# Optimization experiments

Hardware: AMD Instinct MI355X
Metric: run time of the kernel (lower is better)

Reference implementation:

```python
import jax, jax.numpy as jnp
import numpy as np
from jax import lax


def conv(x, w, b, stride, pad):
    # x: [B,C,H,W], w: [O,I,kh,kw] (torch layout)
    y = lax.conv_general_dilated(x, w, (stride, stride), ((pad, pad), (pad, pad)),
                                 dimension_numbers=('NCHW', 'OIHW', 'NCHW'))
    return y + b[None, :, None, None]


def convT(x, w, b, stride, pad):
    # torch ConvTranspose2d weight layout [in, out, kh, kw]
    k = w.shape[2]
    wf = jnp.flip(w, (2, 3)).transpose(1, 0, 2, 3)  # -> [out, in, kh, kw]
    p = k - 1 - pad
    y = lax.conv_general_dilated(x, wf, (1, 1), ((p, p), (p, p)),
                                 lhs_dilation=(stride, stride),
                                 dimension_numbers=('NCHW', 'OIHW', 'NCHW'))
    return y + b[None, :, None, None]


def resblock(x, wa, ba, wb, bb):
    h = conv(jax.nn.relu(x), wa, ba, 1, 1)   # 3x3
    h2 = conv(jax.nn.relu(h), wb, bb, 1, 0)  # 1x1
    return x + h2


def vqvae_forward(x, e1_w, e1_b, e2_w, e2_b, e3_w, e3_b,
                  er1a_w, er1a_b, er1b_w, er1b_b, er2a_w, er2a_b, er2b_w, er2b_b,
                  codebook,
                  d1_w, d1_b, dr1a_w, dr1a_b, dr1b_w, dr1b_b,
                  dr2a_w, dr2a_b, dr2b_w, dr2b_b,
                  dt1_w, dt1_b, dt2_w, dt2_b):
    # encoder
    h = jax.nn.relu(conv(x, e1_w, e1_b, 2, 1))
    h = jax.nn.relu(conv(h, e2_w, e2_b, 2, 1))
    h = conv(h, e3_w, e3_b, 1, 1)
    h = resblock(h, er1a_w, er1a_b, er1b_w, er1b_b)
    ze = resblock(h, er2a_w, er2a_b, er2b_w, er2b_b)  # [B,C,H,W]
    # VQ: nearest codebook vector per spatial location (squared L2)
    zef = ze.transpose(0, 2, 3, 1)  # [B,H,W,C]
    # ||z - e||^2 = ||z||^2 - 2 z.e + ||e||^2 (same argmin as explicit broadcast)
    d = (jnp.sum(zef * zef, -1, keepdims=True)
         - 2.0 * jnp.einsum('bhwc,kc->bhwk', zef, codebook)
         + jnp.sum(codebook * codebook, -1))  # [B,H,W,K]
    idx = jnp.argmin(d, -1)                    # [B,H,W]
    zq = codebook[idx].transpose(0, 3, 1, 2)   # [B,C,H,W]
    # straight-through estimator
    dec_in = ze + lax.stop_gradient(zq - ze)
    # decoder
    g = conv(dec_in, d1_w, d1_b, 1, 1)
    g = resblock(g, dr1a_w, dr1a_b, dr1b_w, dr1b_b)
    g = resblock(g, dr2a_w, dr2a_b, dr2b_w, dr2b_b)
    g = jax.nn.relu(convT(g, dt1_w, dt1_b, 2, 1))
    x_hat = convT(g, dt2_w, dt2_b, 2, 1)
    return x_hat, ze, zq


def setup_inputs() -> dict:
    key = jax.random.key(0)
    ks = iter(jax.random.split(key, 64))
    C, K = 128, 512

    def w(shape, scale=0.02):
        return jax.random.normal(next(ks), shape, jnp.float32) * scale

    inp = {}
    inp['x'] = jax.random.normal(next(ks), (16, 3, 256, 256), jnp.float32)
    inp['e1_w'] = w((C, 3, 4, 4)); inp['e1_b'] = w((C,))
    inp['e2_w'] = w((C, C, 4, 4)); inp['e2_b'] = w((C,))
    inp['e3_w'] = w((C, C, 3, 3)); inp['e3_b'] = w((C,))
    inp['er1a_w'] = w((C, C, 3, 3)); inp['er1a_b'] = w((C,))
    inp['er1b_w'] = w((C, C, 1, 1)); inp['er1b_b'] = w((C,))
    inp['er2a_w'] = w((C, C, 3, 3)); inp['er2a_b'] = w((C,))
    inp['er2b_w'] = w((C, C, 1, 1)); inp['er2b_b'] = w((C,))
    inp['codebook'] = jax.random.uniform(next(ks), (K, C), jnp.float32, -1.0 / K, 1.0 / K)
    inp['d1_w'] = w((C, C, 3, 3)); inp['d1_b'] = w((C,))
    inp['dr1a_w'] = w((C, C, 3, 3)); inp['dr1a_b'] = w((C,))
    inp['dr1b_w'] = w((C, C, 1, 1)); inp['dr1b_b'] = w((C,))
    inp['dr2a_w'] = w((C, C, 3, 3)); inp['dr2a_b'] = w((C,))
    inp['dr2b_w'] = w((C, C, 1, 1)); inp['dr2b_b'] = w((C,))
    inp['dt1_w'] = w((C, C, 4, 4)); inp['dt1_b'] = w((C,))   # ConvTranspose [in,out,kh,kw]
    inp['dt2_w'] = w((C, 3, 4, 4)); inp['dt2_b'] = w((3,))
    return inp


def reference(x, e1_w, e1_b, e2_w, e2_b, e3_w, e3_b,
              er1a_w, er1a_b, er1b_w, er1b_b, er2a_w, er2a_b, er2b_w, er2b_b,
              codebook,
              d1_w, d1_b, dr1a_w, dr1a_b, dr1b_w, dr1b_b,
              dr2a_w, dr2a_b, dr2b_w, dr2b_b,
              dt1_w, dt1_b, dt2_w, dt2_b):
    return vqvae_forward(x, e1_w, e1_b, e2_w, e2_b, e3_w, e3_b,
                         er1a_w, er1a_b, er1b_w, er1b_b, er2a_w, er2a_b, er2b_w, er2b_b,
                         codebook,
                         d1_w, d1_b, dr1a_w, dr1a_b, dr1b_w, dr1b_b,
                         dr2a_w, dr2a_b, dr2b_w, dr2b_b,
                         dt1_w, dt1_b, dt2_w, dt2_b)
```

## Files before the change

### kernel.cpp

```cpp
#include <hip/hip_runtime.h>
#include <stdint.h>

typedef unsigned short u16;
typedef __attribute__((ext_vector_type(8))) short short8;
typedef __attribute__((ext_vector_type(4))) float floatx4;

#define RS66  (66*128)
#define IS66  (66*66*128)
#define RS130 (130*128)
#define IS130 (130*130*128)

__device__ __forceinline__ float bf2f(u16 h) {
  union { unsigned u; float f; } v; v.u = ((unsigned)h) << 16; return v.f;
}
__device__ __forceinline__ u16 f2bf(float f) {
  union { float f; unsigned u; } v; v.f = f;
  unsigned r = v.u + 0x7FFFu + ((v.u >> 16) & 1u);
  return (u16)(r >> 16);
}
__device__ __forceinline__ void gl_lds16(const void* g, void* l) {
  __builtin_amdgcn_global_load_lds(
      (const __attribute__((address_space(1))) void*)(uintptr_t)g,
      (__attribute__((address_space(3))) void*)(uintptr_t)l, 16, 0, 0);
}
__device__ __forceinline__ unsigned fkey(float f) {
  unsigned u = __float_as_uint(f);
  return (u & 0x80000000u) ? ~u : (u | 0x80000000u);
}

struct Taps { int n; unsigned dh2; unsigned dw2; };

__global__ __launch_bounds__(256) void conv_mfma(
    const u16* __restrict__ in, int inRS, int inIS, int si,
    const u16* __restrict__ wt, const float* __restrict__ bias, Taps tp,
    u16* __restrict__ out, int outRS, int outIS, int so, int oh0, int ow0,
    const u16* __restrict__ res, u16* __restrict__ out2, int reluMain,
    float* __restrict__ zeFc, u16* __restrict__ zeBFc, int multi)
{
  __shared__ u16 lA[2][8192];
  __shared__ u16 lB[2][8192];
  const int tid = threadIdx.x;
  const int w = tid >> 6, lane = tid & 63, quad = lane >> 4, l16 = lane & 15;
  const int wm = w >> 1, wn = w & 1;
  const int blockM = blockIdx.x << 7;

  unsigned dh2 = tp.dh2, dw2 = tp.dw2;
  if (multi) {
    const int cls = blockIdx.y;
    dh2 = (tp.dh2 >> (8*cls)) & 0xffu;
    dw2 = (tp.dw2 >> (8*cls)) & 0xffu;
    wt += cls << 16;
    oh0 = cls >> 1; ow0 = cls & 1;
  }

  const int swz = (tid & 7) ^ ((tid >> 3) & 7);
  const u16* gA[4]; const u16* gB[4];
#pragma unroll
  for (int i=0;i<4;i++) {
    const int pg = blockM + i*32 + (tid >> 3);
    const int b = pg >> 12, mo = (pg >> 6) & 63, no = pg & 63;
    gA[i] = in + b*inIS + si*mo*inRS + si*no*128 + swz*8;
    gB[i] = wt + (i*32 + (tid >> 3))*128 + swz*8;
  }
  const int ldsOff = w*512;

  floatx4 zz = {0.f,0.f,0.f,0.f};
  floatx4 acc[4][4];
#pragma unroll
  for (int i=0;i<4;i++)
#pragma unroll
    for (int j=0;j<4;j++) acc[i][j] = zz;

  const int NCH = tp.n << 1;
  auto issue = [&](int ci, int buf) {
    const int t = ci >> 1, kc = ci & 1;
    const int dh = (int)((dh2 >> (2*t)) & 3u) - 1;
    const int dw = (int)((dw2 >> (2*t)) & 3u) - 1;
    const int aoff = dh*inRS + dw*128 + kc*64;
    const int boff = (t << 14) + kc*64;
#pragma unroll
    for (int i=0;i<4;i++) {
      gl_lds16(gA[i] + aoff, &lA[buf][i*2048 + ldsOff]);
      gl_lds16(gB[i] + boff, &lB[buf][i*2048 + ldsOff]);
    }
  };

  issue(0, 0);
  for (int ci = 0; ci < NCH; ++ci) {
    __syncthreads();
    if (ci + 1 < NCH) issue(ci + 1, (ci + 1) & 1);
    const u16* bufA = lA[ci & 1];
    const u16* bufB = lB[ci & 1];
#pragma unroll
    for (int kk=0; kk<2; ++kk) {
      short8 af[4], bfr[4];
#pragma unroll
      for (int s=0;s<4;s++) {
        const int row = wm*64 + s*16 + l16;
        af[s]  = *(const short8*)&bufA[row*64 + (((kk*4 + quad) ^ (l16 & 7)) << 3)];
      }
#pragma unroll
      for (int s=0;s<4;s++) {
        const int row = wn*64 + s*16 + l16;
        bfr[s] = *(const short8*)&bufB[row*64 + (((kk*4 + quad) ^ (l16 & 7)) << 3)];
      }
#pragma unroll
      for (int i=0;i<4;i++)
#pragma unroll
        for (int j=0;j<4;j++)
          acc[i][j] = __builtin_amdgcn_mfma_f32_16x16x32_bf16(af[i], bfr[j], acc[i][j], 0, 0, 0);
    }
  }

  float bv[4];
#pragma unroll
  for (int j=0;j<4;j++) bv[j] = bias[wn*64 + j*16 + l16];

#pragma unroll
  for (int i=0;i<4;i++) {
#pragma unroll
    for (int r=0;r<4;r++) {
      const int p = blockM + wm*64 + i*16 + quad*4 + r;
      const int bb = p >> 12, mo = (p >> 6) & 63, no = p & 63;
      const int ob = bb*outIS + (so*mo + oh0)*outRS + (so*no + ow0)*128;
#pragma unroll
      for (int j=0;j<4;j++) {
        const int n = wn*64 + j*16 + l16;
        float v = acc[i][j][r] + bv[j];
        if (res)  v += bf2f(res[ob + n]);
        if (out)  out[ob + n]  = f2bf(reluMain ? fmaxf(v, 0.f) : v);
        if (out2) out2[ob + n] = f2bf(fmaxf(v, 0.f));
        if (zeFc) {
          zeFc[((size_t)p << 7) + n] = v;
          zeBFc[((size_t)p << 7) + n] = f2bf(v);
        }
      }
    }
  }
}

__global__ __launch_bounds__(256) void vq_score(
    const u16* __restrict__ zeBF, const u16* __restrict__ cbBF,
    const float* __restrict__ cbn, unsigned long long* __restrict__ minbuf)
{
  __shared__ u16 lA[4096];
  __shared__ u16 lB[4096];
  const int tid = threadIdx.x;
  const int w = tid >> 6, lane = tid & 63, quad = lane >> 4, l16 = lane & 15;
  const int wm = w >> 1, wn = w & 1;
  const int q = tid & 3, p0 = tid >> 2;
  const int blockM = blockIdx.x << 7;
  const int nb = blockIdx.y;
  const u16* gA0 = zeBF + ((blockM + p0) << 7) + q*8;
  const u16* gA1 = gA0 + (64 << 7);
  const u16* gB0 = cbBF + ((nb*128 + p0) << 7) + q*8;
  const u16* gB1 = gB0 + (64 << 7);
  u16* lsA0 = lA + w*512; u16* lsA1 = lsA0 + 2048;
  u16* lsB0 = lB + w*512; u16* lsB1 = lsB0 + 2048;

  floatx4 zz = {0.f,0.f,0.f,0.f};
  floatx4 acc[4][4];
#pragma unroll
  for (int i=0;i<4;i++)
#pragma unroll
    for (int j=0;j<4;j++) acc[i][j] = zz;

#pragma unroll
  for (int kc = 0; kc < 4; ++kc) {
    __syncthreads();
    gl_lds16(gA0 + kc*32, lsA0);
    gl_lds16(gA1 + kc*32, lsA1);
    gl_lds16(gB0 + kc*32, lsB0);
    gl_lds16(gB1 + kc*32, lsB1);
    __syncthreads();
    short8 af[4], bfr[4];
#pragma unroll
    for (int s=0;s<4;s++) af[s]  = *(const short8*)&lA[(wm*64 + s*16 + l16)*32 + quad*8];
#pragma unroll
    for (int s=0;s<4;s++) bfr[s] = *(const short8*)&lB[(wn*64 + s*16 + l16)*32 + quad*8];
#pragma unroll
    for (int i=0;i<4;i++)
#pragma unroll
      for (int j=0;j<4;j++)
        acc[i][j] = __builtin_amdgcn_mfma_f32_16x16x32_bf16(af[i], bfr[j], acc[i][j], 0, 0, 0);
  }

  float cn[4];
#pragma unroll
  for (int j=0;j<4;j++) cn[j] = cbn[nb*128 + wn*64 + j*16 + l16];

#pragma unroll
  for (int i=0;i<4;i++) {
#pragma unroll
    for (int r=0;r<4;r++) {
      const int p = blockM + wm*64 + i*16 + quad*4 + r;
      unsigned long long best = 0xFFFFFFFFFFFFFFFFull;
#pragma unroll
      for (int j=0;j<4;j++) {
        const int n = nb*128 + wn*64 + j*16 + l16;
        float v = cn[j] - acc[i][j][r];
        unsigned long long pk = ((unsigned long long)fkey(v) << 32) | (unsigned)n;
        if (pk < best) best = pk;
      }
#pragma unroll
      for (int d=1; d<16; d<<=1) {
        unsigned long long o = __shfl_xor(best, d, 64);
        if (o < best) best = o;
      }
      if (l16 == 0) atomicMin(minbuf + p, best);
    }
  }
}

__global__ __launch_bounds__(256) void finalize(
    const float* __restrict__ zeFc, const unsigned long long* __restrict__ minb,
    const float* __restrict__ cb, float* __restrict__ outZe, float* __restrict__ outZq,
    u16* __restrict__ zqI)
{
  __shared__ float T[64*129];
  __shared__ int ns[64];
  const int tid = threadIdx.x;
  const int P0 = blockIdx.x << 6;
  const int b = P0 >> 12, hw0 = P0 & 4095;

#pragma unroll
  for (int it=0; it<32; ++it) {
    int e = it*256 + tid;
    int px = e >> 7, c = e & 127;
    T[px*129 + c] = zeFc[((size_t)P0 << 7) + e];
  }
  if (tid < 64) ns[tid] = (int)(unsigned)(minb[P0 + tid] & 0xFFFFFFFFull);
  __syncthreads();

  float* zeB = outZe + (((size_t)b) << 19) + hw0;
  float* zqB = outZq + (((size_t)b) << 19) + hw0;
  const int h = hw0 >> 6;
  u16* zqIB = zqI + b*IS66 + h*RS66;
#pragma unroll
  for (int it=0; it<32; ++it) {
    const int c = it*4 + (tid >> 6);
    const int px = tid & 63;
    zeB[(c << 12) + px] = T[px*129 + c];
    float v = cb[(ns[px] << 7) + c];
    zqB[(c << 12) + px] = v;
    zqIB[px*128 + c] = f2bf(v);
  }
}

__global__ __launch_bounds__(256) void zero_halos(
    u16* big, u16* s0, u16* s1, u16* s2, u16* s3, unsigned long long* minb)
{
  int id = blockIdx.x*256 + threadIdx.x;
  if (id >= 463872) return;
  if (id >= 398336) { minb[id - 398336] = 0xFFFFFFFFFFFFFFFFull; return; }
  u16* base; int H, W;
  if (id < 132096) { base = big; H = 128; W = 128; }
  else {
    id -= 132096;
    int bi = id / 66560;
    id -= bi*66560;
    base = (bi == 0) ? s0 : (bi == 1) ? s1 : (bi == 2) ? s2 : s3;
    H = 64; W = 64;
  }
  int Wp = W+2, Hp = H+2;
  int cv = id & 15; int rest = id >> 4;
  int npx = 2*Wp + 2*H;
  int img = rest / npx; int pix = rest - img*npx;
  int hh, wwp;
  if (pix < Wp) { hh = 0; wwp = pix; }
  else if (pix < 2*Wp) { hh = Hp-1; wwp = pix - Wp; }
  else { int r2 = pix - 2*Wp; hh = 1 + (r2 >> 1); wwp = (r2 & 1) ? (Wp-1) : 0; }
  uint4 zv = {0u,0u,0u,0u};
  *(uint4*)(base + (((size_t)img*Hp + hh)*Wp + wwp)*128 + cv*8) = zv;
}

struct WEnt { const float* src; u16* dst; int O, I, T, mode; };
struct WTab { int n; WEnt e[16]; int cum[17]; };
__global__ __launch_bounds__(256) void prep_w(WTab wt) {
  int id = blockIdx.x*256 + threadIdx.x;
  if (id >= wt.cum[wt.n]) return;
  int k = 0;
  while (id >= wt.cum[k+1]) k++;
  int l = id - wt.cum[k];
  WEnt E = wt.e[k];
  if (E.mode == 0) {
    int i = l % E.I; int rest = l / E.I; int o = rest % E.O; int t = rest / E.O;
    E.dst[l] = f2bf(E.src[(o*E.I + i)*E.T + t]);
  } else if (E.mode == 1) {
    int i = l & 127, o = (l >> 7) & 127, tt = (l >> 14) & 3, cls = l >> 16;
    int th = tt >> 1, tw = tt & 1, po = cls >> 1, pw = cls & 1;
    int kh = po ? (th ? 2 : 0) : (th ? 3 : 1);
    int kw = pw ? (tw ? 2 : 0) : (tw ? 3 : 1);
    E.dst[l] = f2bf(E.src[((i*128 + o)*4 + kh)*4 + kw]);
  } else if (E.mode == 2) {
    E.dst[l] = f2bf(E.src[l]);
  } else if (E.mode == 3) {
    float s = 0.f; const float* r = E.src + l*128;
    for (int c=0;c<128;c++) s += r[c]*r[c];
    ((float*)E.dst)[l] = 0.5f*s;
  } else if (E.mode == 4) {
    int o = l & 127, tap = l >> 7;
    ((float*)E.dst)[l] = E.src[o*48 + tap];
  } else {
    int c = l & 127, n = l >> 7;
    int o = n >> 4, kk = n & 15;
    E.dst[l] = f2bf(E.src[c*48 + o*16 + kk]);
  }
}

__global__ __launch_bounds__(256) void conv_e1(
    const float* __restrict__ x, const float* __restrict__ wT,
    const float* __restrict__ bias, u16* __restrict__ outI)
{
  __shared__ float inS[12*260];
  __shared__ float wS[48*128];
  __shared__ float bS[128];
  const int tid = threadIdx.x;
  const int b = blockIdx.x >> 7, ho = blockIdx.x & 127;

  for (int l = tid; l < 1536; l += 256)
    ((float4*)wS)[l] = ((const float4*)wT)[l];
  if (tid < 128) bS[tid] = bias[tid];
  for (int l = tid; l < 3120; l += 256) {
    int col = l % 260; int rest = l / 260;
    int kh = rest & 3, c = rest >> 2;
    int hi = 2*ho + kh - 1, wi = col - 1;
    float v = 0.f;
    if ((unsigned)hi < 256u && (unsigned)wi < 256u)
      v = x[((b*3 + c) << 16) + (hi << 8) + wi];
    inS[rest*260 + col] = v;
  }
  __syncthreads();

  const int g = tid & 7;
  const int pxg = tid >> 3;
  floatx4 acc[4][4];
  {
    const floatx4* bp = (const floatx4*)&bS[g*16];
    floatx4 b0 = bp[0], b1 = bp[1], b2 = bp[2], b3 = bp[3];
#pragma unroll
    for (int px=0;px<4;px++) { acc[px][0]=b0; acc[px][1]=b1; acc[px][2]=b2; acc[px][3]=b3; }
  }
#pragma unroll
  for (int c=0;c<3;c++)
#pragma unroll
    for (int kh=0;kh<4;kh++) {
      const float* row = &inS[(c*4+kh)*260];
#pragma unroll
      for (int kw=0;kw<4;kw++) {
        const int tap = c*16 + kh*4 + kw;
        const floatx4* wp = (const floatx4*)&wS[tap*128 + g*16];
        floatx4 w0 = wp[0], w1 = wp[1], w2 = wp[2], w3 = wp[3];
#pragma unroll
        for (int px=0;px<4;px++) {
          float xv = row[((pxg*4 + px) << 1) + kw];
          acc[px][0] += xv*w0; acc[px][1] += xv*w1;
          acc[px][2] += xv*w2; acc[px][3] += xv*w3;
        }
      }
    }

  u16* ob = outI + b*IS130 + ho*RS130;
#pragma unroll
  for (int px=0;px<4;px++) {
    const int wo = pxg*4 + px;
    u16* p = ob + wo*128 + g*16;
#pragma unroll
    for (int k=0;k<4;k++) {
      union { u16 u[4]; uint2 v2; } pk;
#pragma unroll
      for (int j=0;j<4;j++) pk.u[j] = f2bf(fmaxf(acc[px][k][j], 0.f));
      *(uint2*)(p + k*4) = pk.v2;
    }
  }
}

__global__ __launch_bounds__(256) void dt2_gemm(
    const u16* __restrict__ inI, const u16* __restrict__ Wb,
    float* __restrict__ cols)
{
  const int tid = threadIdx.x;
  const int w = tid >> 6, lane = tid & 63, quad = lane >> 4, l16 = lane & 15;
  const int pixBase = blockIdx.x*256 + w*64;

  short8 Bf[3][4];
#pragma unroll
  for (int nt=0; nt<3; nt++)
#pragma unroll
    for (int kc=0; kc<4; kc++)
      Bf[nt][kc] = *(const short8*)(Wb + (nt*16 + l16)*128 + kc*32 + quad*8);

  const u16* ap[4];
#pragma unroll
  for (int ms=0; ms<4; ms++) {
    int p = pixBase + ms*16 + l16;
    int b = p >> 14, rem = p & 16383;
    ap[ms] = inI + b*IS130 + (rem >> 7)*RS130 + (rem & 127)*128;
  }

  floatx4 zz = {0.f,0.f,0.f,0.f};
  floatx4 acc[4][3];
#pragma unroll
  for (int ms=0; ms<4; ms++)
#pragma unroll
    for (int nt=0; nt<3; nt++) acc[ms][nt] = zz;

#pragma unroll
  for (int kc=0; kc<4; kc++) {
#pragma unroll
    for (int ms=0; ms<4; ms++) {
      short8 a = *(const short8*)(ap[ms] + kc*32 + quad*8);
#pragma unroll
      for (int nt=0; nt<3; nt++)
        acc[ms][nt] = __builtin_amdgcn_mfma_f32_16x16x32_bf16(a, Bf[nt][kc], acc[ms][nt], 0, 0, 0);
    }
  }

#pragma unroll
  for (int ms=0; ms<4; ms++)
#pragma unroll
    for (int nt=0; nt<3; nt++)
#pragma unroll
      for (int r=0; r<4; r++) {
        int p = pixBase + ms*16 + quad*4 + r;
        cols[(size_t)p*48 + nt*16 + l16] = acc[ms][nt][r];
      }
}

__global__ __launch_bounds__(256) void dt2_gather(
    const float* __restrict__ cols, const float* __restrict__ bias,
    float* __restrict__ xhat)
{
  int id = blockIdx.x*256 + threadIdx.x;
  int b = id >> 16, rem = id & 65535;
  int ho = rem >> 8, wo = rem & 255;
  const int ph = ho & 1, pw = wo & 1;
  const int hi0 = ph ? ((ho+1)>>1) : (ho>>1);
  const int kh0 = ph ? 0 : 1;
  const int wi0 = pw ? ((wo+1)>>1) : (wo>>1);
  const int kw0 = pw ? 0 : 1;
  float a0 = bias[0], a1 = bias[1], a2 = bias[2];
#pragma unroll
  for (int th=0; th<2; th++) {
    const int hi = hi0 - th;
    if ((unsigned)hi >= 128u) continue;
    const int kh = kh0 + 2*th;
#pragma unroll
    for (int tw=0; tw<2; tw++) {
      const int wi = wi0 - tw;
      if ((unsigned)wi >= 128u) continue;
      const int kw = kw0 + 2*tw;
      const float* r = cols + (size_t)((b << 14) + (hi << 7) + wi)*48 + (kh*4 + kw);
      a0 += r[0]; a1 += r[16]; a2 += r[32];
    }
  }
  const int ob = ((b*3) << 16) + (ho << 8) + wo;
  xhat[ob]          = a0;
  xhat[ob + 65536]  = a1;
  xhat[ob + 131072] = a2;
}

extern "C" void kernel_launch(void* const* d_in, const int* in_sizes, int n_in,
                              void* d_out, int out_size, void* d_ws, size_t ws_size,
                              hipStream_t stream)
{
  const float* x     = (const float*)d_in[0];
  const float* e1w   = (const float*)d_in[1];
  const float* e1b   = (const float*)d_in[2];
  const float* e2w   = (const float*)d_in[3];
  const float* e2b   = (const float*)d_in[4];
  const float* e3w   = (const float*)d_in[5];
  const float* e3b   = (const float*)d_in[6];
  const float* er1aw = (const float*)d_in[7];
  const float* er1ab = (const float*)d_in[8];
  const float* er1bw = (const float*)d_in[9];
  const float* er1bb = (const float*)d_in[10];
  const float* er2aw = (const float*)d_in[11];
  const float* er2ab = (const float*)d_in[12];
  const float* er2bw = (const float*)d_in[13];
  const float* er2bb = (const float*)d_in[14];
  const float* cb    = (const float*)d_in[15];
  const float* d1w   = (const float*)d_in[16];
  const float* d1b   = (const float*)d_in[17];
  const float* dr1aw = (const float*)d_in[18];
  const float* dr1ab = (const float*)d_in[19];
  const float* dr1bw = (const float*)d_in[20];
  const float* dr1bb = (const float*)d_in[21];
  const float* dr2aw = (const float*)d_in[22];
  const float* dr2ab = (const float*)d_in[23];
  const float* dr2bw = (const float*)d_in[24];
  const float* dr2bb = (const float*)d_in[25];
  const float* dt1w  = (const float*)d_in[26];
  const float* dt1b  = (const float*)d_in[27];
  const float* dt2w  = (const float*)d_in[28];
  const float* dt2b  = (const float*)d_in[29];
  float* out = (float*)d_out;

  char* ws = (char*)d_ws;
  size_t off = 0;
  auto alloc = [&](size_t bytes) -> void* {
    void* r = ws + off; off += (bytes + 255) & ~(size_t)255; return r;
  };

  u16* BIG = (u16*)alloc((size_t)IS130*16*2);
  u16* S[4];
  for (int i=0;i<4;i++) S[i] = (u16*)alloc((size_t)IS66*16*2);
  unsigned long long* minb = (unsigned long long*)alloc((size_t)65536*8);
  u16* W_e2 = (u16*)alloc(262144*2);
  u16* W9[6]; for (int i=0;i<6;i++) W9[i] = (u16*)alloc(147456*2);
  u16* W1[4]; for (int i=0;i<4;i++) W1[i] = (u16*)alloc(16384*2);
  u16* Wdt1 = (u16*)alloc(262144*2);
  u16* cbBF = (u16*)alloc(65536*2);
  float* cbn = (float*)alloc(512*4);
  float* wsE1 = (float*)alloc(6144*4);
  u16* Wb48 = (u16*)alloc(6144*2);

  u16* BIGi = BIG + RS130 + 128;
  u16* Si[4];
  for (int i=0;i<4;i++) Si[i] = S[i] + RS66 + 128;
  u16* zeBFc = S[1];
  float* zeFc = (float*)BIG;
  float* cols = (float*)S[1];

  zero_halos<<<1812, 256, 0, stream>>>(BIG, S[0], S[1], S[2], S[3], minb);

  WTab wtab; int ne = 0; wtab.cum[0] = 0;
  auto addw = [&](const float* s, u16* d, int O, int I, int T, int m, int items) {
    wtab.e[ne] = {s, d, O, I, T, m};
    wtab.cum[ne+1] = wtab.cum[ne] + items; ne++;
  };
  addw(e2w,   W_e2, 128,128,16,0, 262144);
  addw(e3w,   W9[0],128,128, 9,0, 147456);
  addw(er1aw, W9[1],128,128, 9,0, 147456);
  addw(er2aw, W9[2],128,128, 9,0, 147456);
  addw(d1w,   W9[3],128,128, 9,0, 147456);
  addw(dr1aw, W9[4],128,128, 9,0, 147456);
  addw(dr2aw, W9[5],128,128, 9,0, 147456);
  addw(er1bw, W1[0],128,128, 1,0, 16384);
  addw(er2bw, W1[1],128,128, 1,0, 16384);
  addw(dr1bw, W1[2],128,128, 1,0, 16384);
  addw(dr2bw, W1[3],128,128, 1,0, 16384);
  addw(dt1w,  Wdt1, 0,0,0,1, 262144);
  addw(cb,    cbBF, 0,0,0,2, 65536);
  addw(cb,    (u16*)cbn, 0,0,0,3, 512);
  addw(e1w,   (u16*)wsE1, 0,0,0,4, 6144);
  addw(dt2w,  Wb48, 0,0,0,5, 6144);
  wtab.n = ne;
  prep_w<<<(wtab.cum[ne] + 255)/256, 256, 0, stream>>>(wtab);

  conv_e1<<<2048, 256, 0, stream>>>(x, wsE1, e1b, BIGi);

  Taps t16; t16.n = 16; t16.dh2 = 0; t16.dw2 = 0;
  for (int t=0;t<16;t++) { t16.dh2 |= (unsigned)(t>>2) << (2*t); t16.dw2 |= (unsigned)(t&3) << (2*t); }
  Taps t9; t9.n = 9; t9.dh2 = 0; t9.dw2 = 0;
  for (int t=0;t<9;t++) { t9.dh2 |= (unsigned)(t/3) << (2*t); t9.dw2 |= (unsigned)(t%3) << (2*t); }
  Taps t1x; t1x.n = 1; t1x.dh2 = 1; t1x.dw2 = 1;
  Taps tcm; tcm.n = 4; tcm.dh2 = 0; tcm.dw2 = 0;
  for (int cls=0; cls<4; ++cls) {
    int po = cls >> 1, pw = cls & 1;
    for (int tt=0; tt<4; ++tt) {
      int th = tt >> 1, tw = tt & 1;
      int dh = po ? (th ? 0 : 1) : (th ? -1 : 0);
      int dw = pw ? (tw ? 0 : 1) : (tw ? -1 : 0);
      tcm.dh2 |= (unsigned)(dh+1) << (8*cls + 2*tt);
      tcm.dw2 |= (unsigned)(dw+1) << (8*cls + 2*tt);
    }
  }

  auto conv = [&](const u16* in_, int iRS, int iIS, int si,
                  const u16* w_, const float* b_, Taps tp,
                  u16* o_, int oRS, int oIS, int so, int oh, int ow,
                  const u16* r_, u16* o2, int rl, float* zf, u16* zb) {
    conv_mfma<<<512, 256, 0, stream>>>(in_, iRS, iIS, si, w_, b_, tp,
                                       o_, oRS, oIS, so, oh, ow, r_, o2, rl, zf, zb, 0);
  };

  conv(BIGi, RS130, IS130, 2, W_e2, e2b, t16, Si[0], RS66, IS66, 1,0,0, nullptr, nullptr, 1, nullptr, nullptr);
  conv(Si[0], RS66, IS66, 1, W9[0], e3b, t9, Si[1], RS66, IS66, 1,0,0, nullptr, Si[2], 0, nullptr, nullptr);
  conv(Si[2], RS66, IS66, 1, W9[1], er1ab, t9, Si[0], RS66, IS66, 1,0,0, nullptr, nullptr, 1, nullptr, nullptr);
  conv(Si[0], RS66, IS66, 1, W1[0], er1bb, t1x, Si[3], RS66, IS66, 1,0,0, Si[1], Si[2], 0, nullptr, nullptr);
  conv(Si[2], RS66, IS66, 1, W9[2], er2ab, t9, Si[0], RS66, IS66, 1,0,0, nullptr, nullptr, 1, nullptr, nullptr);
  conv(Si[0], RS66, IS66, 1, W1[1], er2bb, t1x, nullptr, RS66, IS66, 1,0,0, Si[3], nullptr, 0, zeFc, zeBFc);

  vq_score<<<dim3(512,4), 256, 0, stream>>>(zeBFc, cbBF, cbn, minb);
  finalize<<<1024, 256, 0, stream>>>(zeFc, minb, cb, out + 3145728, out + 11534336, Si[2]);

  conv(Si[2], RS66, IS66, 1, W9[3], d1b, t9, Si[0], RS66, IS66, 1,0,0, nullptr, Si[1], 0, nullptr, nullptr);
  conv(Si[1], RS66, IS66, 1, W9[4], dr1ab, t9, Si[2], RS66, IS66, 1,0,0, nullptr, nullptr, 1, nullptr, nullptr);
  conv(Si[2], RS66, IS66, 1, W1[2], dr1bb, t1x, Si[3], RS66, IS66, 1,0,0, Si[0], Si[1], 0, nullptr, nullptr);
  conv(Si[1], RS66, IS66, 1, W9[5], dr2ab, t9, Si[2], RS66, IS66, 1,0,0, nullptr, nullptr, 1, nullptr, nullptr);
  conv(Si[2], RS66, IS66, 1, W1[3], dr2bb, t1x, Si[0], RS66, IS66, 1,0,0, Si[3], nullptr, 0, nullptr, nullptr);

  conv_mfma<<<dim3(512,4), 256, 0, stream>>>(Si[0], RS66, IS66, 1, Wdt1, dt1b, tcm,
                                             BIGi, RS130, IS130, 2, 0, 0,
                                             nullptr, nullptr, 1, nullptr, nullptr, 1);

  dt2_gemm<<<1024, 256, 0, stream>>>(BIGi, Wb48, cols);
  dt2_gather<<<4096, 256, 0, stream>>>(cols, dt2b, out);
}
```

Measured before the change: 693.5 us.

## Load MFMA weight fragments directly to registers and swizzle block order

Weights and codebook are pre-packed in prep_w into an MFMA-fragment-ordered layout, so conv_mfma and vq_score read B operands straight from global memory into registers with a software double buffer instead of staging them through LDS. This halves LDS usage, and launch bounds now ask for 3 blocks per CU. Block indices are remapped so that consecutive blocks are spread across distant M tiles, which is meant to improve cache behaviour across CUs. The cost is that every wave fetches B from global or L2 memory on its own, and more registers are in use for the prefetch.

```diff
diff --git a/kernel.cpp b/kernel.cpp
--- a/kernel.cpp
+++ b/kernel.cpp
@@ -30,7 +30,7 @@
 
 struct Taps { int n; unsigned dh2; unsigned dw2; };
 
-__global__ __launch_bounds__(256) void conv_mfma(
+__global__ __launch_bounds__(256, 3) void conv_mfma(
     const u16* __restrict__ in, int inRS, int inIS, int si,
     const u16* __restrict__ wt, const float* __restrict__ bias, Taps tp,
     u16* __restrict__ out, int outRS, int outIS, int so, int oh0, int ow0,
@@ -38,11 +38,11 @@
     float* __restrict__ zeFc, u16* __restrict__ zeBFc, int multi)
 {
   __shared__ u16 lA[2][8192];
-  __shared__ u16 lB[2][8192];
   const int tid = threadIdx.x;
   const int w = tid >> 6, lane = tid & 63, quad = lane >> 4, l16 = lane & 15;
   const int wm = w >> 1, wn = w & 1;
-  const int blockM = blockIdx.x << 7;
+  const int bx = ((blockIdx.x & 7) << 6) | (blockIdx.x >> 3);
+  const int blockM = bx << 7;
 
   unsigned dh2 = tp.dh2, dw2 = tp.dw2;
   if (multi) {
@@ -54,14 +54,14 @@
   }
 
   const int swz = (tid & 7) ^ ((tid >> 3) & 7);
-  const u16* gA[4]; const u16* gB[4];
+  const u16* gA[4];
 #pragma unroll
   for (int i=0;i<4;i++) {
     const int pg = blockM + i*32 + (tid >> 3);
     const int b = pg >> 12, mo = (pg >> 6) & 63, no = pg & 63;
     gA[i] = in + b*inIS + si*mo*inRS + si*no*128 + swz*8;
-    gB[i] = wt + (i*32 + (tid >> 3))*128 + swz*8;
-  }
+  }
+  const u16* gBf = wt + (wn*64 + l16)*32 + quad*8;
   const int ldsOff = w*512;
 
   floatx4 zz = {0.f,0.f,0.f,0.f};
@@ -71,45 +71,46 @@
 #pragma unroll
     for (int j=0;j<4;j++) acc[i][j] = zz;
 
-  const int NCH = tp.n << 1;
-  auto issue = [&](int ci, int buf) {
+  auto issueA = [&](int ci, int buf) {
     const int t = ci >> 1, kc = ci & 1;
     const int dh = (int)((dh2 >> (2*t)) & 3u) - 1;
     const int dw = (int)((dw2 >> (2*t)) & 3u) - 1;
     const int aoff = dh*inRS + dw*128 + kc*64;
-    const int boff = (t << 14) + kc*64;
-#pragma unroll
-    for (int i=0;i<4;i++) {
+#pragma unroll
+    for (int i=0;i<4;i++)
       gl_lds16(gA[i] + aoff, &lA[buf][i*2048 + ldsOff]);
-      gl_lds16(gB[i] + boff, &lB[buf][i*2048 + ldsOff]);
-    }
-  };
-
-  issue(0, 0);
+  };
+  short8 bX[4], bY[4];
+  auto loadB = [&](int ci, int kk, short8 (&b)[4]) {
+    const u16* p = gBf + ci*8192 + kk*4096;
+#pragma unroll
+    for (int s=0;s<4;s++) b[s] = *(const short8*)(p + s*512);
+  };
+  auto computeH = [&](const u16* bufA, int kk, short8 (&bfr)[4]) {
+    short8 af[4];
+#pragma unroll
+    for (int s=0;s<4;s++) {
+      const int row = wm*64 + s*16 + l16;
+      af[s] = *(const short8*)&bufA[row*64 + (((kk*4 + quad) ^ (l16 & 7)) << 3)];
+    }
+#pragma unroll
+    for (int i=0;i<4;i++)
+#pragma unroll
+      for (int j=0;j<4;j++)
+        acc[i][j] = __builtin_amdgcn_mfma_f32_16x16x32_bf16(af[i], bfr[j], acc[i][j], 0, 0, 0);
+  };
+
+  const int NCH = tp.n << 1;
+  loadB(0, 0, bX);
+  issueA(0, 0);
   for (int ci = 0; ci < NCH; ++ci) {
     __syncthreads();
-    if (ci + 1 < NCH) issue(ci + 1, (ci + 1) & 1);
+    if (ci + 1 < NCH) issueA(ci + 1, (ci + 1) & 1);
     const u16* bufA = lA[ci & 1];
-    const u16* bufB = lB[ci & 1];
-#pragma unroll
-    for (int kk=0; kk<2; ++kk) {
-      short8 af[4], bfr[4];
-#pragma unroll
-      for (int s=0;s<4;s++) {
-        const int row = wm*64 + s*16 + l16;
-        af[s]  = *(const short8*)&bufA[row*64 + (((kk*4 + quad) ^ (l16 & 7)) << 3)];
-      }
-#pragma unroll
-      for (int s=0;s<4;s++) {
-        const int row = wn*64 + s*16 + l16;
-        bfr[s] = *(const short8*)&bufB[row*64 + (((kk*4 + quad) ^ (l16 & 7)) << 3)];
-      }
-#pragma unroll
-      for (int i=0;i<4;i++)
-#pragma unroll
-        for (int j=0;j<4;j++)
-          acc[i][j] = __builtin_amdgcn_mfma_f32_16x16x32_bf16(af[i], bfr[j], acc[i][j], 0, 0, 0);
-    }
+    loadB(ci, 1, bY);
+    computeH(bufA, 0, bX);
+    if (ci + 1 < NCH) loadB(ci + 1, 0, bX);
+    computeH(bufA, 1, bY);
   }
 
   float bv[4];
@@ -139,24 +140,24 @@
   }
 }
 
-__global__ __launch_bounds__(256) void vq_score(
-    const u16* __restrict__ zeBF, const u16* __restrict__ cbBF,
+__global__ __launch_bounds__(256, 3) void vq_score(
+    const u16* __restrict__ zeBF, const u16* __restrict__ cbF,
     const float* __restrict__ cbn, unsigned long long* __restrict__ minbuf)
 {
-  __shared__ u16 lA[4096];
-  __shared__ u16 lB[4096];
+  __shared__ u16 lA[2][8192];
   const int tid = threadIdx.x;
   const int w = tid >> 6, lane = tid & 63, quad = lane >> 4, l16 = lane & 15;
   const int wm = w >> 1, wn = w & 1;
-  const int q = tid & 3, p0 = tid >> 2;
-  const int blockM = blockIdx.x << 7;
+  const int bx = ((blockIdx.x & 7) << 6) | (blockIdx.x >> 3);
+  const int blockM = bx << 7;
   const int nb = blockIdx.y;
-  const u16* gA0 = zeBF + ((blockM + p0) << 7) + q*8;
-  const u16* gA1 = gA0 + (64 << 7);
-  const u16* gB0 = cbBF + ((nb*128 + p0) << 7) + q*8;
-  const u16* gB1 = gB0 + (64 << 7);
-  u16* lsA0 = lA + w*512; u16* lsA1 = lsA0 + 2048;
-  u16* lsB0 = lB + w*512; u16* lsB1 = lsB0 + 2048;
+  const int swz = (tid & 7) ^ ((tid >> 3) & 7);
+  const u16* gA[4];
+#pragma unroll
+  for (int i=0;i<4;i++)
+    gA[i] = zeBF + ((size_t)(blockM + i*32 + (tid >> 3)) << 7) + swz*8;
+  const u16* gBf = cbF + (nb << 14) + (wn*64 + l16)*32 + quad*8;
+  const int ldsOff = w*512;
 
   floatx4 zz = {0.f,0.f,0.f,0.f};
   floatx4 acc[4][4];
@@ -165,24 +166,41 @@
 #pragma unroll
     for (int j=0;j<4;j++) acc[i][j] = zz;
 
-#pragma unroll
-  for (int kc = 0; kc < 4; ++kc) {
-    __syncthreads();
-    gl_lds16(gA0 + kc*32, lsA0);
-    gl_lds16(gA1 + kc*32, lsA1);
-    gl_lds16(gB0 + kc*32, lsB0);
-    gl_lds16(gB1 + kc*32, lsB1);
-    __syncthreads();
-    short8 af[4], bfr[4];
-#pragma unroll
-    for (int s=0;s<4;s++) af[s]  = *(const short8*)&lA[(wm*64 + s*16 + l16)*32 + quad*8];
-#pragma unroll
-    for (int s=0;s<4;s++) bfr[s] = *(const short8*)&lB[(wn*64 + s*16 + l16)*32 + quad*8];
+  auto issueA = [&](int kc, int buf) {
+#pragma unroll
+    for (int i=0;i<4;i++)
+      gl_lds16(gA[i] + kc*64, &lA[buf][i*2048 + ldsOff]);
+  };
+  short8 bX[4], bY[4];
+  auto loadB = [&](int ci, int kk, short8 (&b)[4]) {
+    const u16* p = gBf + ci*8192 + kk*4096;
+#pragma unroll
+    for (int s=0;s<4;s++) b[s] = *(const short8*)(p + s*512);
+  };
+  auto computeH = [&](const u16* bufA, int kk, short8 (&bfr)[4]) {
+    short8 af[4];
+#pragma unroll
+    for (int s=0;s<4;s++) {
+      const int row = wm*64 + s*16 + l16;
+      af[s] = *(const short8*)&bufA[row*64 + (((kk*4 + quad) ^ (l16 & 7)) << 3)];
+    }
 #pragma unroll
     for (int i=0;i<4;i++)
 #pragma unroll
       for (int j=0;j<4;j++)
         acc[i][j] = __builtin_amdgcn_mfma_f32_16x16x32_bf16(af[i], bfr[j], acc[i][j], 0, 0, 0);
+  };
+
+  loadB(0, 0, bX);
+  issueA(0, 0);
+  for (int ci = 0; ci < 2; ++ci) {
+    __syncthreads();
+    if (ci == 0) issueA(1, 1);
+    const u16* bufA = lA[ci];
+    loadB(ci, 1, bY);
+    computeH(bufA, 0, bX);
+    if (ci == 0) loadB(1, 0, bX);
+    computeH(bufA, 1, bY);
   }
 
   float cn[4];
@@ -283,17 +301,24 @@
   while (id >= wt.cum[k+1]) k++;
   int l = id - wt.cum[k];
   WEnt E = wt.e[k];
-  if (E.mode == 0) {
-    int i = l % E.I; int rest = l / E.I; int o = rest % E.O; int t = rest / E.O;
-    E.dst[l] = f2bf(E.src[(o*E.I + i)*E.T + t]);
+  if (E.mode == 6) {
+    int e = l & 7, quad = (l >> 3) & 3, row = (l >> 5) & 127;
+    int kk = (l >> 12) & 1, kc = (l >> 13) & 1, t = l >> 14;
+    int i = kc*64 + kk*32 + quad*8 + e;
+    E.dst[l] = f2bf(E.src[(row*E.I + i)*E.T + t]);
   } else if (E.mode == 1) {
-    int i = l & 127, o = (l >> 7) & 127, tt = (l >> 14) & 3, cls = l >> 16;
+    int e = l & 7, quad = (l >> 3) & 3, row = (l >> 5) & 127;
+    int kk = (l >> 12) & 1, kc = (l >> 13) & 1, tt = (l >> 14) & 3, cls = l >> 16;
+    int i = kc*64 + kk*32 + quad*8 + e;
     int th = tt >> 1, tw = tt & 1, po = cls >> 1, pw = cls & 1;
     int kh = po ? (th ? 2 : 0) : (th ? 3 : 1);
     int kw = pw ? (tw ? 2 : 0) : (tw ? 3 : 1);
-    E.dst[l] = f2bf(E.src[((i*128 + o)*4 + kh)*4 + kw]);
-  } else if (E.mode == 2) {
-    E.dst[l] = f2bf(E.src[l]);
+    E.dst[l] = f2bf(E.src[((i*128 + row)*4 + kh)*4 + kw]);
+  } else if (E.mode == 7) {
+    int e = l & 7, quad = (l >> 3) & 3, row = (l >> 5) & 127;
+    int kk = (l >> 12) & 1, kc = (l >> 13) & 1, tt = l >> 14;
+    int i = kc*64 + kk*32 + quad*8 + e;
+    E.dst[l] = f2bf(E.src[(tt*128 + row)*128 + i]);
   } else if (E.mode == 3) {
     float s = 0.f; const float* r = E.src + l*128;
     for (int c=0;c<128;c++) s += r[c]*r[c];
@@ -529,19 +554,19 @@
     wtab.e[ne] = {s, d, O, I, T, m};
     wtab.cum[ne+1] = wtab.cum[ne] + items; ne++;
   };
-  addw(e2w,   W_e2, 128,128,16,0, 262144);
-  addw(e3w,   W9[0],128,128, 9,0, 147456);
-  addw(er1aw, W9[1],128,128, 9,0, 147456);
-  addw(er2aw, W9[2],128,128, 9,0, 147456);
-  addw(d1w,   W9[3],128,128, 9,0, 147456);
-  addw(dr1aw, W9[4],128,128, 9,0, 147456);
-  addw(dr2aw, W9[5],128,128, 9,0, 147456);
-  addw(er1bw, W1[0],128,128, 1,0, 16384);
-  addw(er2bw, W1[1],128,128, 1,0, 16384);
-  addw(dr1bw, W1[2],128,128, 1,0, 16384);
-  addw(dr2bw, W1[3],128,128, 1,0, 16384);
+  addw(e2w,   W_e2, 128,128,16,6, 262144);
+  addw(e3w,   W9[0],128,128, 9,6, 147456);
+  addw(er1aw, W9[1],128,128, 9,6, 147456);
+  addw(er2aw, W9[2],128,128, 9,6, 147456);
+  addw(d1w,   W9[3],128,128, 9,6, 147456);
+  addw(dr1aw, W9[4],128,128, 9,6, 147456);
+  addw(dr2aw, W9[5],128,128, 9,6, 147456);
+  addw(er1bw, W1[0],128,128, 1,6, 16384);
+  addw(er2bw, W1[1],128,128, 1,6, 16384);
+  addw(dr1bw, W1[2],128,128, 1,6, 16384);
+  addw(dr2bw, W1[3],128,128, 1,6, 16384);
   addw(dt1w,  Wdt1, 0,0,0,1, 262144);
-  addw(cb,    cbBF, 0,0,0,2, 65536);
+  addw(cb,    cbBF, 0,0,0,7, 65536);
   addw(cb,    (u16*)cbn, 0,0,0,3, 512);
   addw(e1w,   (u16*)wsE1, 0,0,0,4, 6144);
   addw(dt2w,  Wb48, 0,0,0,5, 6144);
```

After: 730.4 us. 5.3% more time.

## Triple-buffer A tiles with explicit waitcnt pipelining and swizzle block order

Applied to the files above, without the earlier changes.

Splits the global-to-LDS loads of the conv GEMM into separate A and B issues, triple-buffers the activation tile so A is prefetched two chunks ahead, and replaces __syncthreads with explicit vmcnt waits and a raw barrier. It also remaps blockIdx so neighbouring blocks are interleaved across groups of eight, and sets launch bounds to target two blocks per CU. The aim is to hide global load latency and improve cache locality. The cost is extra LDS (a third A buffer), and hand-written waitcnt counts that must match the number of outstanding loads exactly. The remap also assumes the grid size is a multiple of the interleave pattern.

```diff
diff --git a/kernel.cpp b/kernel.cpp
--- a/kernel.cpp
+++ b/kernel.cpp
@@ -30,19 +30,20 @@
 
 struct Taps { int n; unsigned dh2; unsigned dw2; };
 
-__global__ __launch_bounds__(256) void conv_mfma(
+__global__ __launch_bounds__(256, 2) void conv_mfma(
     const u16* __restrict__ in, int inRS, int inIS, int si,
     const u16* __restrict__ wt, const float* __restrict__ bias, Taps tp,
     u16* __restrict__ out, int outRS, int outIS, int so, int oh0, int ow0,
     const u16* __restrict__ res, u16* __restrict__ out2, int reluMain,
     float* __restrict__ zeFc, u16* __restrict__ zeBFc, int multi)
 {
-  __shared__ u16 lA[2][8192];
+  __shared__ u16 lA[3][8192];
   __shared__ u16 lB[2][8192];
   const int tid = threadIdx.x;
   const int w = tid >> 6, lane = tid & 63, quad = lane >> 4, l16 = lane & 15;
   const int wm = w >> 1, wn = w & 1;
-  const int blockM = blockIdx.x << 7;
+  const int bx = ((blockIdx.x & 7) << 6) | (blockIdx.x >> 3);
+  const int blockM = bx << 7;
 
   unsigned dh2 = tp.dh2, dw2 = tp.dw2;
   if (multi) {
@@ -71,26 +72,23 @@
 #pragma unroll
     for (int j=0;j<4;j++) acc[i][j] = zz;
 
-  const int NCH = tp.n << 1;
-  auto issue = [&](int ci, int buf) {
+  auto issueA = [&](int ci, int buf) {
     const int t = ci >> 1, kc = ci & 1;
     const int dh = (int)((dh2 >> (2*t)) & 3u) - 1;
     const int dw = (int)((dw2 >> (2*t)) & 3u) - 1;
     const int aoff = dh*inRS + dw*128 + kc*64;
+#pragma unroll
+    for (int i=0;i<4;i++)
+      gl_lds16(gA[i] + aoff, &lA[buf][i*2048 + ldsOff]);
+  };
+  auto issueB = [&](int ci, int buf) {
+    const int t = ci >> 1, kc = ci & 1;
     const int boff = (t << 14) + kc*64;
 #pragma unroll
-    for (int i=0;i<4;i++) {
-      gl_lds16(gA[i] + aoff, &lA[buf][i*2048 + ldsOff]);
+    for (int i=0;i<4;i++)
       gl_lds16(gB[i] + boff, &lB[buf][i*2048 + ldsOff]);
-    }
   };
-
-  issue(0, 0);
-  for (int ci = 0; ci < NCH; ++ci) {
-    __syncthreads();
-    if (ci + 1 < NCH) issue(ci + 1, (ci + 1) & 1);
-    const u16* bufA = lA[ci & 1];
-    const u16* bufB = lB[ci & 1];
+  auto computeC = [&](const u16* bufA, const u16* bufB) {
 #pragma unroll
     for (int kk=0; kk<2; ++kk) {
       short8 af[4], bfr[4];
@@ -110,6 +108,26 @@
         for (int j=0;j<4;j++)
           acc[i][j] = __builtin_amdgcn_mfma_f32_16x16x32_bf16(af[i], bfr[j], acc[i][j], 0, 0, 0);
     }
+  };
+
+  const int NCH = tp.n << 1;
+  issueA(0, 0);
+  issueB(0, 0);
+  issueA(1, 1);
+  int ab = 0;
+  for (int ci = 0; ci < NCH; ++ci) {
+    if (ci + 1 < NCH) {
+      asm volatile("s_waitcnt vmcnt(4) lgkmcnt(0)" ::: "memory");
+    } else {
+      asm volatile("s_waitcnt vmcnt(0) lgkmcnt(0)" ::: "memory");
+    }
+    __builtin_amdgcn_s_barrier();
+    __builtin_amdgcn_sched_barrier(0);
+    if (ci + 1 < NCH) issueB(ci + 1, (ci + 1) & 1);
+    int a2 = ab + 2; if (a2 >= 3) a2 -= 3;
+    if (ci + 2 < NCH) issueA(ci + 2, a2);
+    computeC(&lA[ab][0], &lB[ci & 1][0]);
+    ab = (ab + 1 == 3) ? 0 : ab + 1;
   }
 
   float bv[4];
```

After: 701.6 us. No clear change (+1.2%).
